# Optimization experiments

Measured on AMD Instinct MI355X. Metric: run time of the kernel, lower is better.

Reference implementation:

```python
import jax, jax.numpy as jnp
import numpy as np

B, T, F, H = 2048, 16, 768, 1024  # batch(nodes), timesteps, 3*input_size, hidden_size


def setup_inputs() -> dict:
    key = jax.random.key(0)
    k1, k2, k3 = jax.random.split(key, 3)
    s_ih = 1.0 / np.sqrt(F)
    s_hh = 1.0 / np.sqrt(H)
    return {
        "x": jax.random.normal(k1, (B, T, F), dtype=jnp.float32),
        "W_ih": jax.random.normal(k2, (F, 4 * H), dtype=jnp.float32) * s_ih,
        "W_hh": jax.random.normal(k3, (H, 4 * H), dtype=jnp.float32) * s_hh,
        "b": jnp.zeros((4 * H,), dtype=jnp.float32),
    }


def reference(x, W_ih, W_hh, b):
    # Batched equivalent of the original per-sample python loop:
    # each sample's [T, F] sequence runs through the LSTM; the final hidden
    # state [H] per sample is concatenated and reshaped to (-1, B).
    Bb, Tt, Ff = x.shape
    Hh = W_hh.shape[0]
    x_t = jnp.swapaxes(x, 0, 1)  # [T, B, F]

    def step(carry, xt):
        h, c = carry
        gates = xt @ W_ih + h @ W_hh + b  # [B, 4H]
        i, f, g, o = jnp.split(gates, 4, axis=-1)
        c = jax.nn.sigmoid(f) * c + jax.nn.sigmoid(i) * jnp.tanh(g)
        h = jax.nn.sigmoid(o) * jnp.tanh(c)
        return (h, c), None

    h0 = jnp.zeros((Bb, Hh), dtype=x.dtype)
    (h, _), _ = jax.lax.scan(step, (h0, h0), x_t)
    # torch.cat over batch of [H] vectors -> flat [B*H], then reshape(-1, B)
    return h.reshape(-1).reshape(-1, Bb)
```

## Files before the change

### kernel.cpp

```cpp
#include <hip/hip_runtime.h>
#include <hip/hip_bf16.h>
#include <stdint.h>

#define B_  2048
#define T_  16
#define F_  768
#define H_  1024
#define G4_ 4096

typedef __attribute__((ext_vector_type(8))) __bf16 bf16x8;
typedef __attribute__((ext_vector_type(4))) float  f32x4;

static __device__ __forceinline__ unsigned short f2bf(float f) {
    union { float f; uint32_t u; } v; v.f = f;
    uint32_t u = v.u;
    uint32_t r = (u + 0x7fffu + ((u >> 16) & 1u)) >> 16;
    return (unsigned short)r;
}
static __device__ __forceinline__ unsigned short f2h(float f) {
    union { _Float16 h; unsigned short u; } v; v.h = (_Float16)f; return v.u;
}
static __device__ __forceinline__ float h2f(unsigned short u) {
    union { _Float16 h; unsigned short u; } v; v.u = u; return (float)v.h;
}
static __device__ __forceinline__ float sigf(float x) {
    return 1.0f / (1.0f + __expf(-x));
}
static __device__ __forceinline__ float tanhfast(float x) {
    return 2.0f / (1.0f + __expf(-2.0f * x)) - 1.0f;
}

#define GLOAD_LDS16(gsrc, ldst)                                                       \
    __builtin_amdgcn_global_load_lds((const __attribute__((address_space(1))) void*)(gsrc), \
                                     (__attribute__((address_space(3))) void*)(ldst), \
                                     16, 0, 0)


__global__ void prep_kernel(const float* __restrict__ x, unsigned short* __restrict__ xbf,
                            const float* __restrict__ Wih, unsigned short* __restrict__ wih_t,
                            const float* __restrict__ Whh, unsigned short* __restrict__ whh_t) {
    const int bid = blockIdx.x;
    const int tid = threadIdx.x;
    if (bid < 24576) {
        int idx = bid * 256 + tid;
        float4 v = *(const float4*)(x + (size_t)idx * 4);
        ushort4 o;
        o.x = f2bf(v.x); o.y = f2bf(v.y); o.z = f2bf(v.z); o.w = f2bf(v.w);
        *(ushort4*)(xbf + (size_t)idx * 4) = o;
        return;
    }
    __shared__ float tile[32][33];
    const float* w;
    unsigned short* wt;
    int K, mode, idx;
    if (bid < 24576 + 3072) { w = Wih; wt = wih_t; K = F_; mode = 0; idx = bid - 24576; }
    else                    { w = Whh; wt = whh_t; K = H_; mode = 1; idx = bid - 27648; }
    int nb = (idx & 127) * 32;
    int kb = (idx >> 7) * 32;
    int tx = tid & 31, ty = tid >> 5;
    #pragma unroll
    for (int i = 0; i < 32; i += 8)
        tile[ty + i][tx] = w[(size_t)(kb + ty + i) * G4_ + nb + tx];
    __syncthreads();
    #pragma unroll
    for (int i = 0; i < 32; i += 8) {
        int n = nb + ty + i;
        int g = n >> 10;
        int j = n & 1023;
        int np = mode ? ((j >> 4) * 64 + g * 16 + (j & 15))
                      : ((j >> 6) * 256 + g * 64 + ((j >> 4) & 3) * 16 + (j & 15));
        wt[(size_t)np * K + kb + tx] = f2bf(tile[tx][ty + i]);
    }
}


#define STAGE4(bufi, kind, half, gbase, ld, rowbase, kt) do {                         \
    const int kel_ = (kt) * 64;                                                       \
    _Pragma("unroll")                                                                 \
    for (int r2 = 0; r2 < 2; ++r2) {                                                  \
        const int rih_ = r2 * 64 + (tid >> 3);                                        \
        const int ch_  = (tid & 7) ^ (rih_ & 7);                                      \
        GLOAD_LDS16((gbase) + (size_t)((rowbase) + (half) * 128 + rih_) * (ld)        \
                            + kel_ + ch_ * 8,                                         \
                    &lds[bufi][kind][half][r2 * 4096 + tid * 8]);                     \
    }                                                                                 \
} while (0)

#define RD4_A(half_, mb)                                                              \
    _Pragma("unroll")                                                                 \
    for (int mm = 0; mm < 4; ++mm) {                                                  \
        const int row_ = ((mb) + mm) * 32 + wm * 16 + fr;                             \
        _Pragma("unroll")                                                             \
        for (int kk = 0; kk < 2; ++kk)                                                \
            Afr[mm][kk] = *(const bf16x8*)&lds[buf][0][half_]                         \
                [(row_ & 127) * 64 + (((kk * 4 + fq) ^ (row_ & 7)) * 8)];             \
    }

#define RD4_B(half_, nb)                                                              \
    _Pragma("unroll")                                                                 \
    for (int nn = 0; nn < 2; ++nn) {                                                  \
        const int row_ = ((nb) + nn) * 64 + wn * 16 + fr;                             \
        _Pragma("unroll")                                                             \
        for (int kk = 0; kk < 2; ++kk)                                                \
            Bfr[(nb) + nn][kk] = *(const bf16x8*)&lds[buf][1][half_]                  \
                [(row_ & 127) * 64 + (((kk * 4 + fq) ^ (row_ & 7)) * 8)];             \
    }

#define MFMAQ(mb, nb)                                                                 \
    __builtin_amdgcn_s_setprio(1);                                                    \
    _Pragma("unroll")                                                                 \
    for (int mm = 0; mm < 4; ++mm)                                                    \
        _Pragma("unroll")                                                             \
        for (int nn = 0; nn < 2; ++nn)                                                \
            _Pragma("unroll")                                                         \
            for (int kk = 0; kk < 2; ++kk)                                            \
                acc[(mb) + mm][(nb) + nn] = __builtin_amdgcn_mfma_f32_16x16x32_bf16(  \
                    Afr[mm][kk], Bfr[(nb) + nn][kk], acc[(mb) + mm][(nb) + nn], 0, 0, 0); \
    __builtin_amdgcn_s_setprio(0);

#define WAITV4  asm volatile("s_waitcnt vmcnt(10)" ::: "memory");                     \
                __builtin_amdgcn_sched_barrier(0);
#define BARR4   __builtin_amdgcn_s_barrier();                                         \
                __builtin_amdgcn_sched_barrier(0);

#define EPIX_M(mbase)                                                                 \
    {                                                                                 \
        _Pragma("unroll")                                                             \
        for (int mm = 0; mm < 8; ++mm) {                                              \
            _Pragma("unroll")                                                         \
            for (int rr = 0; rr < 4; ++rr) {                                          \
                int row_ = (mbase) + mm * 32 + wm * 16 + fq * 4 + rr;                 \
                int tt_ = row_ & 15, bb_ = row_ >> 4;                                 \
                ushort4 o_;                                                           \
                o_.x = f2h(acc[mm][0][rr]);                                           \
                o_.y = f2h(acc[mm][1][rr]);                                           \
                o_.z = f2h(acc[mm][2][rr]);                                           \
                o_.w = f2h(acc[mm][3][rr]);                                           \
                if (tt_ != 0) {                                                       \
                    *(ushort4*)(gx + (((size_t)tt_ * B_ + bb_) * H_ + j) * 4) = o_;   \
                } else {                                                              \
                    float gi_ = bi_ + h2f(o_.x);                                      \
                    float gg_ = bg_ + h2f(o_.z);                                      \
                    float go_ = bo_ + h2f(o_.w);                                      \
                    float cn_ = sigf(gi_) * tanhfast(gg_);                            \
                    float hv_ = sigf(go_) * tanhfast(cn_);                            \
                    size_t off_ = (size_t)bb_ * H_ + j;                               \
                    c[off_] = cn_;                                                    \
                    hbf0[off_] = f2bf(hv_);                                           \
                }                                                                     \
            }                                                                         \
        }                                                                             \
    }

__global__ __launch_bounds__(512, 2) void xgemm8m_kernel(
        const unsigned short* __restrict__ xbf,
        const unsigned short* __restrict__ wih_t,
        unsigned short* __restrict__ gx,
        const float* __restrict__ bias,
        float* __restrict__ c,
        unsigned short* __restrict__ hbf0) {
    __shared__ __align__(16) unsigned short lds[2][2][2][8192];

    const int bid = blockIdx.x;
    const int xcd = bid & 7;
    const int i   = bid >> 3;
    const int bn  = xcd * 2 + (i & 1);
    const int mg  = i >> 1;
    const int bmb = mg * 1024;
    const int bn0 = bn * 256;

    const int tid = threadIdx.x;
    const int wid = tid >> 6, lane = tid & 63;
    const int wm = wid >> 2, wn = wid & 3;
    const int fr = lane & 15, fq = lane >> 4;

    const int j = bn * 64 + wn * 16 + fr;
    float bi_ = 0.f, bg_ = 0.f, bo_ = 0.f;
    if (fq == 0) {
        bi_ = bias[j]; bg_ = bias[2 * H_ + j]; bo_ = bias[3 * H_ + j];
    }

    f32x4 acc[8][4] = {};

    STAGE4(0, 0, 0, xbf, F_, bmb, 0);
    STAGE4(0, 1, 0, wih_t, F_, bn0, 0);
    STAGE4(0, 1, 1, wih_t, F_, bn0, 0);
    STAGE4(0, 0, 1, xbf, F_, bmb, 0);
    STAGE4(1, 0, 0, xbf, F_, bmb, 1);
    STAGE4(1, 1, 0, wih_t, F_, bn0, 1);
    STAGE4(1, 1, 1, wih_t, F_, bn0, 1);
    WAITV4; BARR4;

    for (int kt = 0; kt < 48; ++kt) {
        const int buf = kt & 1, nbuf = buf ^ 1;
        const int k1 = (kt + 1 < 48) ? kt + 1 : 47;
        const int k2 = (kt + 2 < 48) ? kt + 2 : 47;
        const int a1b = bmb + (k1 / 12) * 256, a1k = k1 % 12;
        const int a2b = bmb + (k2 / 12) * 256, a2k = k2 % 12;
        const int b2k = k2 % 12;
        bf16x8 Afr[4][2]; bf16x8 Bfr[4][2];
        RD4_A(0, 0); RD4_B(0, 0);
        STAGE4(nbuf, 0, 1, xbf, F_, a1b, a1k);
        WAITV4; BARR4;
        MFMAQ(0, 0); BARR4;
        RD4_B(1, 2);
        STAGE4(buf, 0, 0, xbf, F_, a2b, a2k);
        WAITV4; BARR4;
        MFMAQ(0, 2); BARR4;
        RD4_A(1, 4);
        STAGE4(buf, 1, 0, wih_t, F_, bn0, b2k);
        BARR4;
        MFMAQ(4, 0); BARR4;
        STAGE4(buf, 1, 1, wih_t, F_, bn0, b2k);
        WAITV4; BARR4;
        MFMAQ(4, 2); BARR4;
        if ((kt % 12) == 11) {
            EPIX_M(bmb + (kt / 12) * 256);
            #pragma unroll
            for (int mm = 0; mm < 8; ++mm)
                #pragma unroll
                for (int nf = 0; nf < 4; ++nf)
                    #pragma unroll
                    for (int q = 0; q < 4; ++q) acc[mm][nf][q] = 0.0f;
        }
    }
}


#define STA6(slot, kt) do {                                                           \
    const int kel_ = (kt) * 64;                                                       \
    _Pragma("unroll")                                                                 \
    for (int r2 = 0; r2 < 2; ++r2) {                                                  \
        const int rih_ = r2 * 32 + (tid >> 3);                                        \
        const int ch_  = (tid & 7) ^ (rih_ & 7);                                      \
        GLOAD_LDS16(hprev + (size_t)(bm0 + rih_) * H_ + kel_ + ch_ * 8,               \
                    &ldsA[slot][r2 * 2048 + tid * 8]);                                \
    }                                                                                 \
} while (0)

#define STB6(slot, rowbase, kt) do {                                                  \
    const int kel_ = (kt) * 64;                                                       \
    _Pragma("unroll")                                                                 \
    for (int r4 = 0; r4 < 4; ++r4) {                                                  \
        const int rih_ = r4 * 32 + (tid >> 3);                                        \
        const int ch_  = (tid & 7) ^ (rih_ & 7);                                      \
        GLOAD_LDS16(whh_t + (size_t)((rowbase) + rih_) * H_ + kel_ + ch_ * 8,         \
                    &ldsB[slot][r4 * 2048 + tid * 8]);                                \
    }                                                                                 \
} while (0)

#define RD_A6(slot, AR)                                                               \
    _Pragma("unroll")                                                                 \
    for (int mm = 0; mm < 2; ++mm) {                                                  \
        const int row_ = wm * 32 + mm * 16 + fr;                                      \
        _Pragma("unroll")                                                             \
        for (int kk = 0; kk < 2; ++kk)                                                \
            AR[mm][kk] = *(const bf16x8*)&ldsA[slot]                                  \
                [row_ * 64 + (((kk * 4 + fq) ^ (row_ & 7)) * 8)];                     \
    }

#define RD_B6(slot, BF)                                                               \
    _Pragma("unroll")                                                                 \
    for (int nf = 0; nf < 4; ++nf) {                                                  \
        const int rowb_ = wn * 64 + nf * 16 + fr;                                     \
        _Pragma("unroll")                                                             \
        for (int kk = 0; kk < 2; ++kk)                                                \
            BF[nf][kk] = *(const bf16x8*)&ldsB[slot]                                  \
                [rowb_ * 64 + (((kk * 4 + fq) ^ (rowb_ & 7)) * 8)];                   \
    }

#define MFMA16S(AR, BF)                                                               \
    __builtin_amdgcn_s_setprio(1);                                                    \
    _Pragma("unroll")                                                                 \
    for (int mm = 0; mm < 2; ++mm)                                                    \
        _Pragma("unroll")                                                             \
        for (int nf = 0; nf < 4; ++nf)                                                \
            _Pragma("unroll")                                                         \
            for (int kk = 0; kk < 2; ++kk)                                            \
                acc[mm][nf] = __builtin_amdgcn_mfma_f32_16x16x32_bf16(                \
                    AR[mm][kk], BF[nf][kk], acc[mm][nf], 0, 0, 0);                    \
    __builtin_amdgcn_s_setprio(0);

#define LGKM0 asm volatile("s_waitcnt lgkmcnt(0)" ::: "memory");
#define BARR  __builtin_amdgcn_s_barrier();

__global__ __launch_bounds__(256, 2) void lstm_step_dp_kernel(
        const unsigned short* __restrict__ hprev,
        const unsigned short* __restrict__ whh_t,
        const unsigned short* __restrict__ gx,
        const float* __restrict__ bias,
        float* __restrict__ c,
        unsigned short* __restrict__ hnext,
        float* __restrict__ hout,
        int t, int last) {
    __shared__ __align__(16) unsigned short ldsA[3][4096];
    __shared__ __align__(16) unsigned short ldsB[3][8192];

    const int bid = blockIdx.x;
    const int xcd = bid & 7;
    const int i   = bid >> 3;
    const int pair = i & 1;
    const int bm  = i >> 1;
    const int bn_base = xcd * 4 + pair * 2;
    const int bm0 = bm * 64;

    const int tid = threadIdx.x;
    const int wid = tid >> 6, lane = tid & 63;
    const int wm = wid >> 1, wn = wid & 1;
    const int fr = lane & 15, fq = lane >> 4;

    const int j0 = (bn_base * 2 + wn) * 16 + fr;
    const int j1 = ((bn_base + 1) * 2 + wn) * 16 + fr;
    const float bi0 = bias[j0], bf0 = bias[H_ + j0], bg0 = bias[2 * H_ + j0], bo0 = bias[3 * H_ + j0];
    const float bi1 = bias[j1], bf1 = bias[H_ + j1], bg1 = bias[2 * H_ + j1], bo1 = bias[3 * H_ + j1];

    f32x4 acc[2][4] = {};
    ushort4 gpre[2][4];
    float   cpre[2][4];

    STA6(0, 0); STB6(0, bn_base * 128, 0);
    STA6(1, 1); STB6(1, bn_base * 128, 1);
    asm volatile("s_waitcnt vmcnt(6)" ::: "memory");
    BARR;

    for (int kt = 0; kt < 32; ++kt) {
        const int s_  = kt % 3;
        const int s2_ = (kt + 2) % 3;
        const int k2  = (kt + 2 < 32) ? kt + 2 : 31;
        const int ak2 = k2 & 15;
        const int brb2 = (bn_base + (k2 >> 4)) * 128;
        bf16x8 Am[2][2], Bf[4][2];
        RD_A6(s_, Am);
        RD_B6(s_, Bf);
        STA6(s2_, ak2);
        STB6(s2_, brb2, ak2);
        if (kt == 13 || kt == 29) {
            const int p_ = kt >> 4;
            const int jp_ = p_ ? j1 : j0;
            #pragma unroll
            for (int mm = 0; mm < 2; ++mm)
                #pragma unroll
                for (int rr = 0; rr < 4; ++rr) {
                    int row_ = bm0 + wm * 32 + mm * 16 + fq * 4 + rr;
                    gpre[mm][rr] = *(const ushort4*)(gx + (((size_t)t * B_ + row_) * H_ + jp_) * 4);
                    cpre[mm][rr] = c[(size_t)row_ * H_ + jp_];
                }
        }
        LGKM0;
        MFMA16S(Am, Bf);
        if (kt == 13 || kt == 14 || kt == 29 || kt == 30)
            asm volatile("s_waitcnt vmcnt(22)" ::: "memory");
        else
            asm volatile("s_waitcnt vmcnt(6)" ::: "memory");
        BARR;
        if (kt == 15) {
            #pragma unroll
            for (int mm = 0; mm < 2; ++mm) {
                #pragma unroll
                for (int rr = 0; rr < 4; ++rr) {
                    int row_ = bm0 + wm * 32 + mm * 16 + fq * 4 + rr;
                    ushort4 g4 = gpre[mm][rr];
                    float gi = acc[mm][0][rr] + bi0 + h2f(g4.x);
                    float gf = acc[mm][1][rr] + bf0 + h2f(g4.y);
                    float gg = acc[mm][2][rr] + bg0 + h2f(g4.z);
                    float go = acc[mm][3][rr] + bo0 + h2f(g4.w);
                    float cn = sigf(gf) * cpre[mm][rr] + sigf(gi) * tanhfast(gg);
                    float hv = sigf(go) * tanhfast(cn);
                    size_t off = (size_t)row_ * H_ + j0;
                    c[off] = cn;
                    hnext[off] = f2bf(hv);
                    if (last) hout[off] = hv;
                }
            }
            #pragma unroll
            for (int mm = 0; mm < 2; ++mm)
                #pragma unroll
                for (int nf = 0; nf < 4; ++nf)
                    #pragma unroll
                    for (int q = 0; q < 4; ++q) acc[mm][nf][q] = 0.0f;
        }
    }

    #pragma unroll
    for (int mm = 0; mm < 2; ++mm) {
        #pragma unroll
        for (int rr = 0; rr < 4; ++rr) {
            int row_ = bm0 + wm * 32 + mm * 16 + fq * 4 + rr;
            ushort4 g4 = gpre[mm][rr];
            float gi = acc[mm][0][rr] + bi1 + h2f(g4.x);
            float gf = acc[mm][1][rr] + bf1 + h2f(g4.y);
            float gg = acc[mm][2][rr] + bg1 + h2f(g4.z);
            float go = acc[mm][3][rr] + bo1 + h2f(g4.w);
            float cn = sigf(gf) * cpre[mm][rr] + sigf(gi) * tanhfast(gg);
            float hv = sigf(go) * tanhfast(cn);
            size_t off = (size_t)row_ * H_ + j1;
            c[off] = cn;
            hnext[off] = f2bf(hv);
            if (last) hout[off] = hv;
        }
    }
}


extern "C" void kernel_launch(void* const* d_in, const int* in_sizes, int n_in,
                              void* d_out, int out_size, void* d_ws, size_t ws_size,
                              hipStream_t stream) {
    const float* x    = (const float*)d_in[0];
    const float* Wih  = (const float*)d_in[1];
    const float* Whh  = (const float*)d_in[2];
    const float* bias = (const float*)d_in[3];
    float* out = (float*)d_out;

    char* ws = (char*)d_ws;
    unsigned short* xbf   = (unsigned short*)(ws);
    unsigned short* wih_t = (unsigned short*)(ws + 50331648);
    unsigned short* whh_t = (unsigned short*)(ws + 56623104);
    unsigned short* hbf0  = (unsigned short*)(ws + 65011712);
    unsigned short* hbf1  = (unsigned short*)(ws + 69206016);
    float*          c     = (float*)(ws + 73400320);
    unsigned short* gx    = (unsigned short*)(ws + 81788928);

    hipLaunchKernelGGL(prep_kernel, dim3(24576 + 3072 + 4096), dim3(256), 0, stream,
                       x, xbf, Wih, wih_t, Whh, whh_t);

    hipLaunchKernelGGL(xgemm8m_kernel, dim3(512), dim3(512), 0, stream,
                       xbf, wih_t, gx, bias, c, hbf0);

    for (int t = 1; t < T_; ++t) {
        unsigned short* hr = (t & 1) ? hbf0 : hbf1;
        unsigned short* hw = (t & 1) ? hbf1 : hbf0;
        hipLaunchKernelGGL(lstm_step_dp_kernel, dim3(512), dim3(256), 0, stream,
                           hr, whh_t, gx, bias, c, hw, out, t, (t == T_ - 1) ? 1 : 0);
    }
}
```

Before: 724.9 us.

## Retile recurrent step kernel to 128x128 tiles with BK=32 pipeline

Replaces the 64-row x two-128-column-tile recurrent step (BK=64, K swept twice) with a single 128x128 output tile per block and a BK=32 K-loop over all 1024 hidden elements. Each block now stages A and B at 32 columns each with a 4-chunk XOR swizzle, doing 16 MFMAs per stage, and runs one epilogue at the end. The larger square tile raises arithmetic intensity and halves the B-operand LDS footprint. In exchange it doubles the accumulator and prefetch register arrays (acc, gpre, cpre) and shortens each K-step, which may pressure occupancy at 2 waves per SIMD and add barrier overhead.

```diff
diff --git a/kernel.cpp b/kernel.cpp
--- a/kernel.cpp
+++ b/kernel.cpp
@@ -227,64 +227,58 @@
 }
 
 
-#define STA6(slot, kt) do {                                                           \
-    const int kel_ = (kt) * 64;                                                       \
+#define STG_A32(slot, kt) do {                                                        \
+    const int kel_ = (kt) * 32;                                                       \
     _Pragma("unroll")                                                                 \
     for (int r2 = 0; r2 < 2; ++r2) {                                                  \
-        const int rih_ = r2 * 32 + (tid >> 3);                                        \
-        const int ch_  = (tid & 7) ^ (rih_ & 7);                                      \
+        const int rih_ = r2 * 64 + (tid >> 2);                                        \
+        const int ch_  = (tid & 3) ^ ((rih_ >> 2) & 3);                               \
         GLOAD_LDS16(hprev + (size_t)(bm0 + rih_) * H_ + kel_ + ch_ * 8,               \
                     &ldsA[slot][r2 * 2048 + tid * 8]);                                \
     }                                                                                 \
 } while (0)
 
-#define STB6(slot, rowbase, kt) do {                                                  \
-    const int kel_ = (kt) * 64;                                                       \
-    _Pragma("unroll")                                                                 \
-    for (int r4 = 0; r4 < 4; ++r4) {                                                  \
-        const int rih_ = r4 * 32 + (tid >> 3);                                        \
-        const int ch_  = (tid & 7) ^ (rih_ & 7);                                      \
-        GLOAD_LDS16(whh_t + (size_t)((rowbase) + rih_) * H_ + kel_ + ch_ * 8,         \
-                    &ldsB[slot][r4 * 2048 + tid * 8]);                                \
+#define STG_B32(slot, kt) do {                                                        \
+    const int kel_ = (kt) * 32;                                                       \
+    _Pragma("unroll")                                                                 \
+    for (int r2 = 0; r2 < 2; ++r2) {                                                  \
+        const int rih_ = r2 * 64 + (tid >> 2);                                        \
+        const int ch_  = (tid & 3) ^ ((rih_ >> 2) & 3);                               \
+        GLOAD_LDS16(whh_t + (size_t)(bn0 + rih_) * H_ + kel_ + ch_ * 8,               \
+                    &ldsB[slot][r2 * 2048 + tid * 8]);                                \
     }                                                                                 \
 } while (0)
 
-#define RD_A6(slot, AR)                                                               \
-    _Pragma("unroll")                                                                 \
-    for (int mm = 0; mm < 2; ++mm) {                                                  \
-        const int row_ = wm * 32 + mm * 16 + fr;                                      \
-        _Pragma("unroll")                                                             \
-        for (int kk = 0; kk < 2; ++kk)                                                \
-            AR[mm][kk] = *(const bf16x8*)&ldsA[slot]                                  \
-                [row_ * 64 + (((kk * 4 + fq) ^ (row_ & 7)) * 8)];                     \
-    }
-
-#define RD_B6(slot, BF)                                                               \
+#define RD_A32(slot, AR)                                                              \
+    _Pragma("unroll")                                                                 \
+    for (int mm = 0; mm < 4; ++mm) {                                                  \
+        const int row_ = wm * 64 + mm * 16 + fr;                                      \
+        AR[mm] = *(const bf16x8*)&ldsA[slot]                                          \
+            [row_ * 32 + ((fq ^ ((row_ >> 2) & 3)) * 8)];                             \
+    }
+
+#define RD_B32(slot, BF)                                                              \
     _Pragma("unroll")                                                                 \
     for (int nf = 0; nf < 4; ++nf) {                                                  \
-        const int rowb_ = wn * 64 + nf * 16 + fr;                                     \
-        _Pragma("unroll")                                                             \
-        for (int kk = 0; kk < 2; ++kk)                                                \
-            BF[nf][kk] = *(const bf16x8*)&ldsB[slot]                                  \
-                [rowb_ * 64 + (((kk * 4 + fq) ^ (rowb_ & 7)) * 8)];                   \
-    }
-
-#define MFMA16S(AR, BF)                                                               \
+        const int row_ = wn * 64 + nf * 16 + fr;                                      \
+        BF[nf] = *(const bf16x8*)&ldsB[slot]                                          \
+            [row_ * 32 + ((fq ^ ((row_ >> 2) & 3)) * 8)];                             \
+    }
+
+#define MFMA16T(AR, BF)                                                               \
     __builtin_amdgcn_s_setprio(1);                                                    \
     _Pragma("unroll")                                                                 \
-    for (int mm = 0; mm < 2; ++mm)                                                    \
+    for (int mm = 0; mm < 4; ++mm)                                                    \
         _Pragma("unroll")                                                             \
         for (int nf = 0; nf < 4; ++nf)                                                \
-            _Pragma("unroll")                                                         \
-            for (int kk = 0; kk < 2; ++kk)                                            \
-                acc[mm][nf] = __builtin_amdgcn_mfma_f32_16x16x32_bf16(                \
-                    AR[mm][kk], BF[nf][kk], acc[mm][nf], 0, 0, 0);                    \
+            acc[mm][nf] = __builtin_amdgcn_mfma_f32_16x16x32_bf16(                    \
+                AR[mm], BF[nf], acc[mm][nf], 0, 0, 0);                                \
     __builtin_amdgcn_s_setprio(0);
 
 #define LGKM0 asm volatile("s_waitcnt lgkmcnt(0)" ::: "memory");
 #define BARR  __builtin_amdgcn_s_barrier();
 
-__global__ __launch_bounds__(256, 2) void lstm_step_dp_kernel(
+__global__ __launch_bounds__(256, 2) void lstm_step32_kernel(
         const unsigned short* __restrict__ hprev,
         const unsigned short* __restrict__ whh_t,
         const unsigned short* __restrict__ gx,
@@ -294,106 +288,77 @@
         float* __restrict__ hout,
         int t, int last) {
     __shared__ __align__(16) unsigned short ldsA[3][4096];
-    __shared__ __align__(16) unsigned short ldsB[3][8192];
+    __shared__ __align__(16) unsigned short ldsB[3][4096];
 
     const int bid = blockIdx.x;
     const int xcd = bid & 7;
     const int i   = bid >> 3;
-    const int pair = i & 1;
-    const int bm  = i >> 1;
-    const int bn_base = xcd * 4 + pair * 2;
-    const int bm0 = bm * 64;
+    const int bn  = xcd * 4 + (i & 3);
+    const int bm  = i >> 2;
+    const int bm0 = bm * 128, bn0 = bn * 128;
 
     const int tid = threadIdx.x;
     const int wid = tid >> 6, lane = tid & 63;
     const int wm = wid >> 1, wn = wid & 1;
     const int fr = lane & 15, fq = lane >> 4;
 
-    const int j0 = (bn_base * 2 + wn) * 16 + fr;
-    const int j1 = ((bn_base + 1) * 2 + wn) * 16 + fr;
-    const float bi0 = bias[j0], bf0 = bias[H_ + j0], bg0 = bias[2 * H_ + j0], bo0 = bias[3 * H_ + j0];
-    const float bi1 = bias[j1], bf1 = bias[H_ + j1], bg1 = bias[2 * H_ + j1], bo1 = bias[3 * H_ + j1];
-
-    f32x4 acc[2][4] = {};
-    ushort4 gpre[2][4];
-    float   cpre[2][4];
-
-    STA6(0, 0); STB6(0, bn_base * 128, 0);
-    STA6(1, 1); STB6(1, bn_base * 128, 1);
-    asm volatile("s_waitcnt vmcnt(6)" ::: "memory");
+    const int j = (bn * 2 + wn) * 16 + fr;
+    const float bi = bias[j];
+    const float bf = bias[H_ + j];
+    const float bg = bias[2 * H_ + j];
+    const float bo = bias[3 * H_ + j];
+
+    f32x4 acc[4][4] = {};
+    ushort4 gpre[4][4];
+    float   cpre[4][4];
+
+    STG_A32(0, 0); STG_B32(0, 0);
+    STG_A32(1, 1); STG_B32(1, 1);
+    asm volatile("s_waitcnt vmcnt(4)" ::: "memory");
     BARR;
 
     for (int kt = 0; kt < 32; ++kt) {
         const int s_  = kt % 3;
         const int s2_ = (kt + 2) % 3;
-        const int k2  = (kt + 2 < 32) ? kt + 2 : 31;
-        const int ak2 = k2 & 15;
-        const int brb2 = (bn_base + (k2 >> 4)) * 128;
-        bf16x8 Am[2][2], Bf[4][2];
-        RD_A6(s_, Am);
-        RD_B6(s_, Bf);
-        STA6(s2_, ak2);
-        STB6(s2_, brb2, ak2);
-        if (kt == 13 || kt == 29) {
-            const int p_ = kt >> 4;
-            const int jp_ = p_ ? j1 : j0;
+        const int k2_ = (kt + 2 < 32) ? kt + 2 : 31;
+        bf16x8 Am[4], Bf[4];
+        RD_A32(s_, Am);
+        RD_B32(s_, Bf);
+        STG_A32(s2_, k2_);
+        STG_B32(s2_, k2_);
+        if (kt == 29) {
             #pragma unroll
-            for (int mm = 0; mm < 2; ++mm)
+            for (int mm = 0; mm < 4; ++mm)
                 #pragma unroll
                 for (int rr = 0; rr < 4; ++rr) {
-                    int row_ = bm0 + wm * 32 + mm * 16 + fq * 4 + rr;
-                    gpre[mm][rr] = *(const ushort4*)(gx + (((size_t)t * B_ + row_) * H_ + jp_) * 4);
-                    cpre[mm][rr] = c[(size_t)row_ * H_ + jp_];
+                    int row_ = bm0 + wm * 64 + mm * 16 + fq * 4 + rr;
+                    gpre[mm][rr] = *(const ushort4*)(gx + (((size_t)t * B_ + row_) * H_ + j) * 4);
+                    cpre[mm][rr] = c[(size_t)row_ * H_ + j];
                 }
         }
         LGKM0;
-        MFMA16S(Am, Bf);
-        if (kt == 13 || kt == 14 || kt == 29 || kt == 30)
-            asm volatile("s_waitcnt vmcnt(22)" ::: "memory");
+        MFMA16T(Am, Bf);
+        if (kt >= 29)
+            asm volatile("s_waitcnt vmcnt(36)" ::: "memory");
         else
-            asm volatile("s_waitcnt vmcnt(6)" ::: "memory");
+            asm volatile("s_waitcnt vmcnt(4)" ::: "memory");
         BARR;
-        if (kt == 15) {
-            #pragma unroll
-            for (int mm = 0; mm < 2; ++mm) {
-                #pragma unroll
-                for (int rr = 0; rr < 4; ++rr) {
-                    int row_ = bm0 + wm * 32 + mm * 16 + fq * 4 + rr;
-                    ushort4 g4 = gpre[mm][rr];
-                    float gi = acc[mm][0][rr] + bi0 + h2f(g4.x);
-                    float gf = acc[mm][1][rr] + bf0 + h2f(g4.y);
-                    float gg = acc[mm][2][rr] + bg0 + h2f(g4.z);
-                    float go = acc[mm][3][rr] + bo0 + h2f(g4.w);
-                    float cn = sigf(gf) * cpre[mm][rr] + sigf(gi) * tanhfast(gg);
-                    float hv = sigf(go) * tanhfast(cn);
-                    size_t off = (size_t)row_ * H_ + j0;
-                    c[off] = cn;
-                    hnext[off] = f2bf(hv);
-                    if (last) hout[off] = hv;
-                }
-            }
-            #pragma unroll
-            for (int mm = 0; mm < 2; ++mm)
-                #pragma unroll
-                for (int nf = 0; nf < 4; ++nf)
-                    #pragma unroll
-                    for (int q = 0; q < 4; ++q) acc[mm][nf][q] = 0.0f;
-        }
-    }
+    }
+    asm volatile("s_waitcnt vmcnt(0)" ::: "memory");
 
     #pragma unroll
-    for (int mm = 0; mm < 2; ++mm) {
+    for (int mm = 0; mm < 4; ++mm) {
         #pragma unroll
         for (int rr = 0; rr < 4; ++rr) {
-            int row_ = bm0 + wm * 32 + mm * 16 + fq * 4 + rr;
+            int row_ = bm0 + wm * 64 + mm * 16 + fq * 4 + rr;
             ushort4 g4 = gpre[mm][rr];
-            float gi = acc[mm][0][rr] + bi1 + h2f(g4.x);
-            float gf = acc[mm][1][rr] + bf1 + h2f(g4.y);
-            float gg = acc[mm][2][rr] + bg1 + h2f(g4.z);
-            float go = acc[mm][3][rr] + bo1 + h2f(g4.w);
+            float gi = acc[mm][0][rr] + bi + h2f(g4.x);
+            float gf = acc[mm][1][rr] + bf + h2f(g4.y);
+            float gg = acc[mm][2][rr] + bg + h2f(g4.z);
+            float go = acc[mm][3][rr] + bo + h2f(g4.w);
             float cn = sigf(gf) * cpre[mm][rr] + sigf(gi) * tanhfast(gg);
             float hv = sigf(go) * tanhfast(cn);
-            size_t off = (size_t)row_ * H_ + j1;
+            size_t off = (size_t)row_ * H_ + j;
             c[off] = cn;
             hnext[off] = f2bf(hv);
             if (last) hout[off] = hv;
@@ -429,7 +394,7 @@
     for (int t = 1; t < T_; ++t) {
         unsigned short* hr = (t & 1) ? hbf0 : hbf1;
         unsigned short* hw = (t & 1) ? hbf1 : hbf0;
-        hipLaunchKernelGGL(lstm_step_dp_kernel, dim3(512), dim3(256), 0, stream,
+        hipLaunchKernelGGL(lstm_step32_kernel, dim3(512), dim3(256), 0, stream,
                            hr, whh_t, gx, bias, c, hw, out, t, (t == T_ - 1) ? 1 : 0);
     }
 }
```

Result: slower. 837.1 us (+15.5%).
